# Kernel optimization log

Hardware: AMD Instinct MI355X
Metric: run time of the kernel (lower is better)

The kernel has to match this reference:

```python
import jax, jax.numpy as jnp
import numpy as np

B, S, D, H = 4, 2048, 512, 8
DEPTH = D // H
BAND = 16  # log_thresholds [1,2,4,8,16] union == distance <= 16


def setup_inputs() -> dict:
    key = jax.random.key(0)
    ks = jax.random.split(key, 11)
    sc = 0.02
    return {
        "q": jax.random.normal(ks[0], (B, S, D), jnp.float32),
        "k": jax.random.normal(ks[1], (B, S, D), jnp.float32),
        "v": jax.random.normal(ks[2], (B, S, D), jnp.float32),
        "wq": jax.random.normal(ks[3], (D, D), jnp.float32) * sc,
        "bq": jnp.zeros((D,), jnp.float32),
        "wk": jax.random.normal(ks[4], (D, D), jnp.float32) * sc,
        "bk": jnp.zeros((D,), jnp.float32),
        "wv": jax.random.normal(ks[5], (D, D), jnp.float32) * sc,
        "bv": jnp.zeros((D,), jnp.float32),
        "wo": jax.random.normal(ks[6], (D, D), jnp.float32) * sc,
        "bo": jnp.zeros((D,), jnp.float32),
    }


def _split_heads(x):
    # [B,S,D] -> [B,H,S,depth]
    b, s, _ = x.shape
    return x.reshape(b, s, H, DEPTH).transpose(0, 2, 1, 3)


def reference(q, k, v, wq, bq, wk, bk, wv, bv, wo, bo):
    qh = _split_heads(q @ wq + bq)
    kh = _split_heads(k @ wk + bk)
    vh = _split_heads(v @ wv + bv)
    scale = 1.0 / jnp.sqrt(jnp.float32(DEPTH))
    logits = jnp.einsum("bhqd,bhkd->bhqk", qh, kh) * scale  # [B,H,S,S]
    idx = jnp.arange(S)
    keep = jnp.abs(idx[:, None] - idx[None, :]) <= BAND  # band mask [S,S]
    logits = jnp.where(keep[None, None], logits, jnp.float32(-1e9))
    attn = jax.nn.softmax(logits, axis=-1)
    out = jnp.einsum("bhqk,bhkd->bhqd", attn, vh)
    out = out.transpose(0, 2, 1, 3).reshape(q.shape[0], -1, D)
    return out @ wo + bo
```

## Files before the change

kernel.cpp:

```cpp
#include <hip/hip_runtime.h>

typedef unsigned int uint;
typedef unsigned short ushort;
typedef __attribute__((ext_vector_type(8))) short bf16x8;
typedef __attribute__((ext_vector_type(4))) float f32x4;

namespace {
constexpr int kS = 2048;
constexpr int kD = 512;
constexpr int kH = 8;
constexpr int kNT = 8192;
constexpr int kBand = 16;
}

static __device__ __forceinline__ ushort f2bf(float f) {
  uint u = __builtin_bit_cast(uint, f);
  u = (u + 0x7fffu + ((u >> 16) & 1u)) >> 16;
  return (ushort)u;
}

#define GLD16(gp, lp)                                                   \
  __builtin_amdgcn_global_load_lds(                                     \
      (const __attribute__((address_space(1))) uint*)(gp),              \
      (__attribute__((address_space(3))) uint*)(lp), 16, 0, 0)

__global__ __launch_bounds__(256) void prep_kernel(
    const float* __restrict__ q, const float* __restrict__ k,
    const float* __restrict__ v, const float* __restrict__ wq,
    const float* __restrict__ wk, const float* __restrict__ wv,
    const float* __restrict__ wo, ushort* __restrict__ qb,
    ushort* __restrict__ kb, ushort* __restrict__ vb,
    ushort* __restrict__ WT) {
  __shared__ float Ws[64][65];
  const int blk = blockIdx.x;
  const int tid = threadIdx.x;
  if (blk < 6144) {
    const int z = blk >> 11, t = blk & 2047;
    const float* src = z == 0 ? q : (z == 1 ? k : v);
    ushort* dst = z == 0 ? qb : (z == 1 ? kb : vb);
    const size_t i8 = ((size_t)t * 256 + tid) * 8;
    const float4 x0 = *(const float4*)(src + i8);
    const float4 x1 = *(const float4*)(src + i8 + 4);
    alignas(16) ushort t8[8] = {f2bf(x0.x), f2bf(x0.y), f2bf(x0.z), f2bf(x0.w),
                                f2bf(x1.x), f2bf(x1.y), f2bf(x1.z), f2bf(x1.w)};
    *(uint4*)(dst + i8) = *(const uint4*)t8;
    return;
  }
  const int w = blk - 6144;
  const int z = w >> 6;
  const float* W = z == 0 ? wq : (z == 1 ? wk : (z == 2 ? wv : wo));
  ushort* T = WT + (size_t)z * kD * kD;
  const int kt = ((w >> 3) & 7) * 64, nt = (w & 7) * 64;
  const int r = tid >> 2, c0 = (tid & 3) * 16;
#pragma unroll
  for (int i = 0; i < 4; ++i) {
    const float4 x =
        *(const float4*)(W + (size_t)(kt + r) * kD + nt + c0 + i * 4);
    Ws[r][c0 + i * 4 + 0] = x.x;
    Ws[r][c0 + i * 4 + 1] = x.y;
    Ws[r][c0 + i * 4 + 2] = x.z;
    Ws[r][c0 + i * 4 + 3] = x.w;
  }
  __syncthreads();
  const int n = tid >> 2, k0 = (tid & 3) * 16;
  alignas(16) ushort tmp[16];
#pragma unroll
  for (int i = 0; i < 16; ++i) tmp[i] = f2bf(Ws[k0 + i][n]);
  ushort* dst = T + (size_t)(nt + n) * kD + kt + k0;
  *(uint4*)(dst + 0) = *(const uint4*)&tmp[0];
  *(uint4*)(dst + 8) = *(const uint4*)&tmp[8];
}

template <int TM>
__global__ __launch_bounds__(256) void gemm_kernel(
    const ushort* __restrict__ qb, const ushort* __restrict__ kb,
    const ushort* __restrict__ vb, const ushort* __restrict__ obp,
    const ushort* __restrict__ WT, const float* __restrict__ bq,
    const float* __restrict__ bk, const float* __restrict__ bv,
    const float* __restrict__ bo, ushort* __restrict__ Qp,
    ushort* __restrict__ Kp, ushort* __restrict__ VT,
    float* __restrict__ outp, int mode_arg) {
  const int mode = mode_arg + blockIdx.z;
  const ushort* Ab;
  const float* bias;
  switch (mode) {
    case 0: Ab = qb; bias = bq; break;
    case 1: Ab = kb; bias = bk; break;
    case 2: Ab = vb; bias = bv; break;
    default: Ab = obp; bias = bo; break;
  }
  const ushort* BT = WT + (size_t)mode * kD * kD;

  constexpr int A_STAGE = TM * 32;
  constexpr int B_BASE = 3 * A_STAGE;
  constexpr int NI = (TM == 128) ? 4 : 2;
  constexpr int AI = TM / 64;
  __shared__ alignas(16) ushort smem[B_BASE + 12288];

  const int tid = threadIdx.x;
  const int wave = tid >> 6, lane = tid & 63, l15 = lane & 15, qd = lane >> 4;
  const int wm = (TM == 128) ? (wave >> 1) * 64 : 0;
  const int wn = (TM == 128) ? (wave & 1) * 64 : wave * 32;
  const int lin = blockIdx.x;
  const int xcd = lin & 7, j = lin >> 3;
  const int rblk = xcd + 8 * (j >> 2), cblk = j & 3;
  const int row0 = rblk * TM, col0 = cblk * 128;
  const int sw = (l15 & 3) ^ (l15 >> 2);

  const ushort* pA[AI];
  const ushort* pB[2];
  uint ldsA[AI], ldsB[2];
#pragma unroll
  for (int i = 0; i < AI; ++i) {
    const int linear = i * 256 + tid;
    const int r = linear >> 2, c = linear & 3;
    const int g = c ^ ((r & 3) ^ ((r >> 2) & 3));
    pA[i] = Ab + (size_t)(row0 + r) * kD + g * 8;
    ldsA[i] = (uint)(i * 256 + wave * 64) * 8;
  }
#pragma unroll
  for (int i = 0; i < 2; ++i) {
    const int linear = i * 256 + tid;
    const int r = linear >> 2, c = linear & 3;
    const int g = c ^ ((r & 3) ^ ((r >> 2) & 3));
    pB[i] = BT + (size_t)(col0 + r) * kD + g * 8;
    ldsB[i] = (uint)B_BASE + (uint)(i * 256 + wave * 64) * 8;
  }

#define ISSUE(kk, st)                                                     \
  {                                                                       \
    _Pragma("unroll") for (int i = 0; i < AI; ++i)                        \
        GLD16(pA[i] + (kk), &smem[ldsA[i] + (st) * A_STAGE]);             \
    _Pragma("unroll") for (int i = 0; i < 2; ++i)                         \
        GLD16(pB[i] + (kk), &smem[ldsB[i] + (st) * 4096]);                \
  }

  f32x4 acc[4][NI];
#pragma unroll
  for (int mi = 0; mi < 4; ++mi)
#pragma unroll
    for (int ni = 0; ni < NI; ++ni) acc[mi][ni] = (f32x4)(0.f);

  ISSUE(0, 0);
  ISSUE(32, 1);
#pragma unroll
  for (int it = 0; it < 16; ++it) {
    if (it < 15) {
      if constexpr (TM == 128)
        asm volatile("s_waitcnt vmcnt(4) lgkmcnt(0)\n\ts_barrier" ::: "memory");
      else
        asm volatile("s_waitcnt vmcnt(3) lgkmcnt(0)\n\ts_barrier" ::: "memory");
    } else {
      asm volatile("s_waitcnt vmcnt(0) lgkmcnt(0)\n\ts_barrier" ::: "memory");
    }
    if (it < 14) ISSUE((it + 2) * 32, (it + 2) % 3);
    const ushort* as = &smem[(it % 3) * A_STAGE];
    const ushort* bs = &smem[B_BASE + (it % 3) * 4096];
    bf16x8 af[4], br[NI];
#pragma unroll
    for (int mi = 0; mi < 4; ++mi)
      af[mi] = *(const bf16x8*)&as[(wm + mi * 16 + l15) * 32 + (qd ^ sw) * 8];
#pragma unroll
    for (int ni = 0; ni < NI; ++ni)
      br[ni] = *(const bf16x8*)&bs[(wn + ni * 16 + l15) * 32 + (qd ^ sw) * 8];
#pragma unroll
    for (int mi = 0; mi < 4; ++mi)
#pragma unroll
      for (int ni = 0; ni < NI; ++ni)
        acc[mi][ni] = __builtin_amdgcn_mfma_f32_16x16x32_bf16(
            af[mi], br[ni], acc[mi][ni], 0, 0, 0);
  }
#undef ISSUE

  float bcol[NI];
#pragma unroll
  for (int ni = 0; ni < NI; ++ni) bcol[ni] = bias[col0 + wn + ni * 16 + l15];

  if (mode == 3) {
#pragma unroll
    for (int mi = 0; mi < 4; ++mi)
#pragma unroll
      for (int ni = 0; ni < NI; ++ni) {
        const int n_g = col0 + wn + ni * 16 + l15;
#pragma unroll
        for (int r = 0; r < 4; ++r) {
          const int token = row0 + wm + mi * 16 + qd * 4 + r;
          outp[(size_t)token * kD + n_g] = acc[mi][ni][r] + bcol[ni];
        }
      }
    return;
  }

  __syncthreads();

  ushort* T = &smem[wave * 4608];
  if (mode <= 1) {
#pragma unroll
    for (int mi = 0; mi < 4; ++mi)
#pragma unroll
      for (int ni = 0; ni < NI; ++ni)
#pragma unroll
        for (int r = 0; r < 4; ++r)
          T[(mi * 16 + qd * 4 + r) * 72 + ni * 16 + l15] =
              f2bf(acc[mi][ni][r] + bcol[ni]);
  } else {
#pragma unroll
    for (int mi = 0; mi < 4; ++mi)
#pragma unroll
      for (int ni = 0; ni < NI; ++ni)
#pragma unroll
        for (int r = 0; r < 4; ++r)
          T[(ni * 16 + l15) * 72 + mi * 16 + qd * 4 + r] =
              f2bf(acc[mi][ni][r] + bcol[ni]);
  }
  asm volatile("s_waitcnt lgkmcnt(0)" ::: "memory");

  const ushort* Trow = &smem[wave * 4608 + lane * 72];
  if (mode <= 1) {
    ushort* C = (mode == 0) ? Qp : Kp;
    ushort* dst = C + (size_t)(row0 + wm + lane) * kD + col0 + wn;
#pragma unroll
    for (int c = 0; c < 8; ++c)
      *(uint4*)(dst + c * 8) = *(const uint4*)(Trow + c * 8);
  } else {
    const int n_g = col0 + wn + lane;
    const int h = n_g >> 6, d = n_g & 63;
    const int t0 = row0 + wm;
    const int b = t0 >> 11, ss = t0 & (kS - 1);
    ushort* dst = VT + ((size_t)(b * kH + h) * 64 + d) * kS + ss;
#pragma unroll
    for (int c = 0; c < 8; ++c)
      *(uint4*)(dst + c * 8) = *(const uint4*)(Trow + c * 8);
  }
}

__global__ __launch_bounds__(64, 1) void attn_kernel(
    const ushort* __restrict__ Qp, const ushort* __restrict__ Kp,
    const ushort* __restrict__ VT, ushort* __restrict__ Ob) {
  __shared__ alignas(16) ushort Pl[64 * 104];

  const int lane = threadIdx.x, l15 = lane & 15, qd = lane >> 4;
  const int bh = blockIdx.y, b = bh >> 3, h = bh & 7;
  const int q0 = blockIdx.x * 64;
  const int colA = h * 64;

  bf16x8 qf[4][2], kf[6][2];
#pragma unroll
  for (int mi = 0; mi < 4; ++mi) {
    const size_t base =
        ((size_t)b * kS + q0 + mi * 16 + l15) * kD + colA + qd * 8;
#pragma unroll
    for (int kc = 0; kc < 2; ++kc)
      qf[mi][kc] = *(const bf16x8*)&Qp[base + kc * 32];
  }
#pragma unroll
  for (int ni = 0; ni < 6; ++ni) {
    int key = q0 - kBand + ni * 16 + l15;
    key = key < 0 ? 0 : (key > kS - 1 ? kS - 1 : key);
    const size_t base = ((size_t)b * kS + key) * kD + colA + qd * 8;
#pragma unroll
    for (int kc = 0; kc < 2; ++kc)
      kf[ni][kc] = *(const bf16x8*)&Kp[base + kc * 32];
  }

  f32x4 S[4][6];
#pragma unroll
  for (int mi = 0; mi < 4; ++mi)
#pragma unroll
    for (int ni = 0; ni < 6; ++ni) S[mi][ni] = (f32x4)(0.f);
#pragma unroll
  for (int mi = 0; mi < 4; ++mi)
#pragma unroll
    for (int ni = 0; ni < 6; ++ni)
#pragma unroll
      for (int kc = 0; kc < 2; ++kc)
        S[mi][ni] = __builtin_amdgcn_mfma_f32_16x16x32_bf16(
            qf[mi][kc], kf[ni][kc], S[mi][ni], 0, 0, 0);

#pragma unroll
  for (int mi = 0; mi < 4; ++mi)
#pragma unroll
    for (int ni = 0; ni < 6; ++ni)
#pragma unroll
      for (int r = 0; r < 4; ++r) {
        const int q_local = mi * 16 + qd * 4 + r;
        const int key_local = ni * 16 + l15;
        const int key = q0 - kBand + key_local;
        const int dlt = key_local - q_local;
        const bool ok = (dlt >= 0) && (dlt <= 32) && (key >= 0) && (key < kS);
        S[mi][ni][r] = ok ? S[mi][ni][r] * 0.125f : -3.0e38f;
      }

  float inv[4][4];
#pragma unroll
  for (int mi = 0; mi < 4; ++mi)
#pragma unroll
    for (int r = 0; r < 4; ++r) {
      float m = S[mi][0][r];
#pragma unroll
      for (int ni = 1; ni < 6; ++ni) m = fmaxf(m, S[mi][ni][r]);
      m = fmaxf(m, __shfl_xor(m, 1));
      m = fmaxf(m, __shfl_xor(m, 2));
      m = fmaxf(m, __shfl_xor(m, 4));
      m = fmaxf(m, __shfl_xor(m, 8));
      float s = 0.f;
#pragma unroll
      for (int ni = 0; ni < 6; ++ni) {
        const float e = __expf(S[mi][ni][r] - m);
        S[mi][ni][r] = e;
        s += e;
      }
      s += __shfl_xor(s, 1);
      s += __shfl_xor(s, 2);
      s += __shfl_xor(s, 4);
      s += __shfl_xor(s, 8);
      inv[mi][r] = 1.f / s;
    }

#pragma unroll
  for (int mi = 0; mi < 4; ++mi)
#pragma unroll
    for (int ni = 0; ni < 6; ++ni)
#pragma unroll
      for (int r = 0; r < 4; ++r)
        Pl[(mi * 16 + qd * 4 + r) * 104 + ni * 16 + l15] = f2bf(S[mi][ni][r]);
  __syncthreads();

  f32x4 O[4][4];
#pragma unroll
  for (int mi = 0; mi < 4; ++mi)
#pragma unroll
    for (int nt = 0; nt < 4; ++nt) O[mi][nt] = (f32x4)(0.f);

#pragma unroll
  for (int kc = 0; kc < 3; ++kc) {
    bf16x8 pf[4], vfr[4];
#pragma unroll
    for (int mi = 0; mi < 4; ++mi)
      pf[mi] = *(const bf16x8*)&Pl[(mi * 16 + l15) * 104 + kc * 32 + qd * 8];
    int kb0 = q0 - kBand + kc * 32 + qd * 8;
    kb0 = kb0 < 0 ? 0 : (kb0 > kS - 8 ? kS - 8 : kb0);
#pragma unroll
    for (int nt = 0; nt < 4; ++nt)
      vfr[nt] =
          *(const bf16x8*)&VT[((size_t)bh * 64 + nt * 16 + l15) * kS + kb0];
#pragma unroll
    for (int mi = 0; mi < 4; ++mi)
#pragma unroll
      for (int nt = 0; nt < 4; ++nt)
        O[mi][nt] = __builtin_amdgcn_mfma_f32_16x16x32_bf16(pf[mi], vfr[nt],
                                                            O[mi][nt], 0, 0, 0);
  }

#pragma unroll
  for (int mi = 0; mi < 4; ++mi)
#pragma unroll
    for (int nt = 0; nt < 4; ++nt)
#pragma unroll
      for (int r = 0; r < 4; ++r)
        Pl[(mi * 16 + qd * 4 + r) * 72 + nt * 16 + l15] =
            f2bf(O[mi][nt][r] * inv[mi][r]);
  asm volatile("s_waitcnt lgkmcnt(0)" ::: "memory");

  ushort* dst = Ob + ((size_t)b * kS + q0 + lane) * kD + colA;
  const ushort* Trow = &Pl[lane * 72];
#pragma unroll
  for (int c = 0; c < 8; ++c)
    *(uint4*)(dst + c * 8) = *(const uint4*)(Trow + c * 8);
}

extern "C" void kernel_launch(void* const* d_in, const int* in_sizes, int n_in,
                              void* d_out, int out_size, void* d_ws,
                              size_t ws_size, hipStream_t stream) {
  const float* q = (const float*)d_in[0];
  const float* k = (const float*)d_in[1];
  const float* v = (const float*)d_in[2];
  const float* wq = (const float*)d_in[3];
  const float* bq = (const float*)d_in[4];
  const float* wk = (const float*)d_in[5];
  const float* bk = (const float*)d_in[6];
  const float* wv = (const float*)d_in[7];
  const float* bv = (const float*)d_in[8];
  const float* wo = (const float*)d_in[9];
  const float* bo = (const float*)d_in[10];
  float* out = (float*)d_out;

  const size_t n1 = (size_t)kNT * kD;
  ushort* qb = (ushort*)d_ws;
  ushort* kb = qb + n1;
  ushort* vb = kb + n1;
  ushort* Qp = vb + n1;
  ushort* Kp = Qp + n1;
  ushort* VT = Kp + n1;
  ushort* Ob = VT + n1;
  ushort* WT = Ob + n1;

  prep_kernel<<<dim3(6400), 256, 0, stream>>>(q, k, v, wq, wk, wv, wo, qb, kb,
                                              vb, WT);
  gemm_kernel<128><<<dim3(256, 1, 3), 256, 0, stream>>>(
      qb, kb, vb, Ob, WT, bq, bk, bv, bo, Qp, Kp, VT, out, 0);
  attn_kernel<<<dim3(kS / 64, 32), 64, 0, stream>>>(Qp, Kp, VT, Ob);
  gemm_kernel<64><<<dim3(512, 1, 1), 256, 0, stream>>>(
      qb, kb, vb, Ob, WT, bq, bk, bv, bo, Qp, Kp, VT, out, 3);
}
```

Before: 158.4 us.

## Fuse fp32-to-bf16 activation conversion into QKV projection GEMM loads

Result: slower. 163.7 us (+3.4%).

```diff
diff --git a/kernel.cpp b/kernel.cpp
--- a/kernel.cpp
+++ b/kernel.cpp
@@ -9,8 +9,10 @@
 constexpr int kS = 2048;
 constexpr int kD = 512;
 constexpr int kH = 8;
-constexpr int kNT = 8192;
 constexpr int kBand = 16;
+
+template <bool C, typename A, typename B> struct cond { using type = A; };
+template <typename A, typename B> struct cond<false, A, B> { using type = B; };
 }
 
 static __device__ __forceinline__ ushort f2bf(float f) {
@@ -19,34 +21,27 @@
   return (ushort)u;
 }
 
+static __device__ __forceinline__ bf16x8 cvt8(f32x4 lo, f32x4 hi) {
+  uint4 r;
+  asm("v_cvt_pk_bf16_f32 %0, %1, %2" : "=v"(r.x) : "v"(lo[0]), "v"(lo[1]));
+  asm("v_cvt_pk_bf16_f32 %0, %1, %2" : "=v"(r.y) : "v"(lo[2]), "v"(lo[3]));
+  asm("v_cvt_pk_bf16_f32 %0, %1, %2" : "=v"(r.z) : "v"(hi[0]), "v"(hi[1]));
+  asm("v_cvt_pk_bf16_f32 %0, %1, %2" : "=v"(r.w) : "v"(hi[2]), "v"(hi[3]));
+  return __builtin_bit_cast(bf16x8, r);
+}
+
 #define GLD16(gp, lp)                                                   \
   __builtin_amdgcn_global_load_lds(                                     \
       (const __attribute__((address_space(1))) uint*)(gp),              \
       (__attribute__((address_space(3))) uint*)(lp), 16, 0, 0)
 
 __global__ __launch_bounds__(256) void prep_kernel(
-    const float* __restrict__ q, const float* __restrict__ k,
-    const float* __restrict__ v, const float* __restrict__ wq,
-    const float* __restrict__ wk, const float* __restrict__ wv,
-    const float* __restrict__ wo, ushort* __restrict__ qb,
-    ushort* __restrict__ kb, ushort* __restrict__ vb,
+    const float* __restrict__ wq, const float* __restrict__ wk,
+    const float* __restrict__ wv, const float* __restrict__ wo,
     ushort* __restrict__ WT) {
   __shared__ float Ws[64][65];
-  const int blk = blockIdx.x;
+  const int w = blockIdx.x;
   const int tid = threadIdx.x;
-  if (blk < 6144) {
-    const int z = blk >> 11, t = blk & 2047;
-    const float* src = z == 0 ? q : (z == 1 ? k : v);
-    ushort* dst = z == 0 ? qb : (z == 1 ? kb : vb);
-    const size_t i8 = ((size_t)t * 256 + tid) * 8;
-    const float4 x0 = *(const float4*)(src + i8);
-    const float4 x1 = *(const float4*)(src + i8 + 4);
-    alignas(16) ushort t8[8] = {f2bf(x0.x), f2bf(x0.y), f2bf(x0.z), f2bf(x0.w),
-                                f2bf(x1.x), f2bf(x1.y), f2bf(x1.z), f2bf(x1.w)};
-    *(uint4*)(dst + i8) = *(const uint4*)t8;
-    return;
-  }
-  const int w = blk - 6144;
   const int z = w >> 6;
   const float* W = z == 0 ? wq : (z == 1 ? wk : (z == 2 ? wv : wo));
   ushort* T = WT + (size_t)z * kD * kD;
@@ -71,30 +66,32 @@
   *(uint4*)(dst + 8) = *(const uint4*)&tmp[8];
 }
 
-template <int TM>
+template <int TM, bool AF32>
 __global__ __launch_bounds__(256) void gemm_kernel(
-    const ushort* __restrict__ qb, const ushort* __restrict__ kb,
-    const ushort* __restrict__ vb, const ushort* __restrict__ obp,
+    const float* __restrict__ qf, const float* __restrict__ kf,
+    const float* __restrict__ vf, const ushort* __restrict__ obp,
     const ushort* __restrict__ WT, const float* __restrict__ bq,
     const float* __restrict__ bk, const float* __restrict__ bv,
     const float* __restrict__ bo, ushort* __restrict__ Qp,
     ushort* __restrict__ Kp, ushort* __restrict__ VT,
     float* __restrict__ outp, int mode_arg) {
   const int mode = mode_arg + blockIdx.z;
-  const ushort* Ab;
+  const void* Abv;
   const float* bias;
   switch (mode) {
-    case 0: Ab = qb; bias = bq; break;
-    case 1: Ab = kb; bias = bk; break;
-    case 2: Ab = vb; bias = bv; break;
-    default: Ab = obp; bias = bo; break;
-  }
+    case 0: Abv = qf; bias = bq; break;
+    case 1: Abv = kf; bias = bk; break;
+    case 2: Abv = vf; bias = bv; break;
+    default: Abv = obp; bias = bo; break;
+  }
+  using AT = typename cond<AF32, float, ushort>::type;
+  const AT* Abt = (const AT*)Abv;
   const ushort* BT = WT + (size_t)mode * kD * kD;
 
-  constexpr int A_STAGE = TM * 32;
+  constexpr int A_STAGE = TM * (AF32 ? 64 : 32);
   constexpr int B_BASE = 3 * A_STAGE;
   constexpr int NI = (TM == 128) ? 4 : 2;
-  constexpr int AI = TM / 64;
+  constexpr int AI = AF32 ? TM / 32 : TM / 64;
   __shared__ alignas(16) ushort smem[B_BASE + 12288];
 
   const int tid = threadIdx.x;
@@ -107,15 +104,21 @@
   const int row0 = rblk * TM, col0 = cblk * 128;
   const int sw = (l15 & 3) ^ (l15 >> 2);
 
-  const ushort* pA[AI];
+  const AT* pA[AI];
   const ushort* pB[2];
   uint ldsA[AI], ldsB[2];
 #pragma unroll
   for (int i = 0; i < AI; ++i) {
     const int linear = i * 256 + tid;
-    const int r = linear >> 2, c = linear & 3;
-    const int g = c ^ ((r & 3) ^ ((r >> 2) & 3));
-    pA[i] = Ab + (size_t)(row0 + r) * kD + g * 8;
+    int r, g;
+    if constexpr (AF32) {
+      r = linear >> 3;
+      g = (linear & 7) ^ (r & 7);
+    } else {
+      r = linear >> 2;
+      g = (linear & 3) ^ ((r & 3) ^ ((r >> 2) & 3));
+    }
+    pA[i] = Abt + (size_t)(row0 + r) * kD + g * (AF32 ? 4 : 8);
     ldsA[i] = (uint)(i * 256 + wave * 64) * 8;
   }
 #pragma unroll
@@ -146,20 +149,34 @@
 #pragma unroll
   for (int it = 0; it < 16; ++it) {
     if (it < 15) {
-      if constexpr (TM == 128)
-        asm volatile("s_waitcnt vmcnt(4) lgkmcnt(0)\n\ts_barrier" ::: "memory");
-      else
+      if constexpr (AI + 2 == 6) {
+        asm volatile("s_waitcnt vmcnt(6) lgkmcnt(0)\n\ts_barrier" ::: "memory");
+      } else {
+        static_assert(AI + 2 == 3 || AI + 2 == 6, "unexpected stage size");
         asm volatile("s_waitcnt vmcnt(3) lgkmcnt(0)\n\ts_barrier" ::: "memory");
+      }
     } else {
       asm volatile("s_waitcnt vmcnt(0) lgkmcnt(0)\n\ts_barrier" ::: "memory");
     }
     if (it < 14) ISSUE((it + 2) * 32, (it + 2) % 3);
-    const ushort* as = &smem[(it % 3) * A_STAGE];
+    bf16x8 af[4], br[NI];
+    if constexpr (AF32) {
+      const float* as = (const float*)&smem[(it % 3) * A_STAGE];
+#pragma unroll
+      for (int mi = 0; mi < 4; ++mi) {
+        const int row = wm + mi * 16 + l15;
+        const int s2 = l15 & 7;
+        const f32x4 lo = *(const f32x4*)&as[row * 32 + ((2 * qd) ^ s2) * 4];
+        const f32x4 hi = *(const f32x4*)&as[row * 32 + ((2 * qd + 1) ^ s2) * 4];
+        af[mi] = cvt8(lo, hi);
+      }
+    } else {
+      const ushort* as = &smem[(it % 3) * A_STAGE];
+#pragma unroll
+      for (int mi = 0; mi < 4; ++mi)
+        af[mi] = *(const bf16x8*)&as[(wm + mi * 16 + l15) * 32 + (qd ^ sw) * 8];
+    }
     const ushort* bs = &smem[B_BASE + (it % 3) * 4096];
-    bf16x8 af[4], br[NI];
-#pragma unroll
-    for (int mi = 0; mi < 4; ++mi)
-      af[mi] = *(const bf16x8*)&as[(wm + mi * 16 + l15) * 32 + (qd ^ sw) * 8];
 #pragma unroll
     for (int ni = 0; ni < NI; ++ni)
       br[ni] = *(const bf16x8*)&bs[(wn + ni * 16 + l15) * 32 + (qd ^ sw) * 8];
@@ -385,21 +402,17 @@
   const float* bo = (const float*)d_in[10];
   float* out = (float*)d_out;
 
-  const size_t n1 = (size_t)kNT * kD;
-  ushort* qb = (ushort*)d_ws;
-  ushort* kb = qb + n1;
-  ushort* vb = kb + n1;
-  ushort* Qp = vb + n1;
+  const size_t n1 = (size_t)8192 * kD;
+  ushort* Qp = (ushort*)d_ws;
   ushort* Kp = Qp + n1;
   ushort* VT = Kp + n1;
   ushort* Ob = VT + n1;
   ushort* WT = Ob + n1;
 
-  prep_kernel<<<dim3(6400), 256, 0, stream>>>(q, k, v, wq, wk, wv, wo, qb, kb,
-                                              vb, WT);
-  gemm_kernel<128><<<dim3(256, 1, 3), 256, 0, stream>>>(
-      qb, kb, vb, Ob, WT, bq, bk, bv, bo, Qp, Kp, VT, out, 0);
+  prep_kernel<<<dim3(256), 256, 0, stream>>>(wq, wk, wv, wo, WT);
+  gemm_kernel<128, true><<<dim3(256, 1, 3), 256, 0, stream>>>(
+      q, k, v, Ob, WT, bq, bk, bv, bo, Qp, Kp, VT, out, 0);
   attn_kernel<<<dim3(kS / 64, 32), 64, 0, stream>>>(Qp, Kp, VT, Ob);
-  gemm_kernel<64><<<dim3(512, 1, 1), 256, 0, stream>>>(
-      qb, kb, vb, Ob, WT, bq, bk, bv, bo, Qp, Kp, VT, out, 3);
-}
+  gemm_kernel<64, false><<<dim3(512, 1, 1), 256, 0, stream>>>(
+      q, k, v, Ob, WT, bq, bk, bv, bo, Qp, Kp, VT, out, 3);
+}
```
